# Kernel tuning notes

Measured on AMD Instinct MI355X. Metric: run time of the kernel, lower is better.

## Reference

```python
import jax, jax.numpy as jnp
import numpy as np

ASPECT_RATIOS = jnp.array([0.5, 1.0, 2.0], dtype=jnp.float32)
SCALES = jnp.array([1.0, 2.0, 4.0, 8.0, 16.0], dtype=jnp.float32)
BASE_SIZE = 16
STRIDE = 16
NEG_OVERLAP = 0.3
POS_OVERLAP = 0.7
PADDING = 0.0
RPN_BATCH = 256
RPN_FG_FRACTION = 0.5


def _mkanchors(ws, hs, x_ctr, y_ctr):
    return jnp.stack([x_ctr - 0.5 * (ws - 1), y_ctr - 0.5 * (hs - 1),
                      x_ctr + 0.5 * (ws - 1), y_ctr + 0.5 * (hs - 1)], axis=-1)


def _base_anchors():
    w = h = float(BASE_SIZE)
    x_ctr = y_ctr = 0.5 * (BASE_SIZE - 1)
    size = w * h
    size_ratios = size / ASPECT_RATIOS
    ws = jnp.round(jnp.sqrt(size_ratios))
    hs = jnp.round(ws * ASPECT_RATIOS)
    ratio_anchors = _mkanchors(ws, hs, x_ctr, y_ctr)          # (R,4)
    rw = ratio_anchors[:, 2] - ratio_anchors[:, 0] + 1
    rh = ratio_anchors[:, 3] - ratio_anchors[:, 1] + 1
    rx = ratio_anchors[:, 0] + 0.5 * (rw - 1)
    ry = ratio_anchors[:, 1] + 0.5 * (rh - 1)
    ws2 = rw[:, None] * SCALES[None, :]                        # (R,S)
    hs2 = rh[:, None] * SCALES[None, :]
    anchors = _mkanchors(ws2, hs2, rx[:, None], ry[:, None])   # (R,S,4)
    return anchors.reshape(-1, 4)                              # (A=R*S,4)


def _shifted_anchors(r, c):
    base = _base_anchors()                                     # (A,4)
    sx = jnp.arange(c, dtype=jnp.float32) * STRIDE
    sy = jnp.arange(r, dtype=jnp.float32) * STRIDE
    SX, SY = jnp.meshgrid(sx, sy)                              # (r,c)
    shifts = jnp.stack([SX.ravel(), SY.ravel(), SX.ravel(), SY.ravel()], axis=1)
    return (shifts[:, None, :] + base[None, :, :]).reshape(-1, 4)  # (K=r*c*A,4)


def _iou(a, b):
    area_a = (a[:, 2] - a[:, 0] + 1) * (a[:, 3] - a[:, 1] + 1)
    area_b = (b[:, 2] - b[:, 0] + 1) * (b[:, 3] - b[:, 1] + 1)
    iw = jnp.minimum(a[:, None, 2], b[None, :, 2]) - jnp.maximum(a[:, None, 0], b[None, :, 0]) + 1
    ih = jnp.minimum(a[:, None, 3], b[None, :, 3]) - jnp.maximum(a[:, None, 1], b[None, :, 1]) + 1
    inter = jnp.maximum(iw, 0) * jnp.maximum(ih, 0)
    return inter / (area_a[:, None] + area_b[None, :] - inter)


def _bbox_transform(ex, gt):
    ew = ex[:, 2] - ex[:, 0] + 1.0
    eh = ex[:, 3] - ex[:, 1] + 1.0
    ecx = ex[:, 0] + 0.5 * ew
    ecy = ex[:, 1] + 0.5 * eh
    gw = gt[:, 2] - gt[:, 0] + 1.0
    gh = gt[:, 3] - gt[:, 1] + 1.0
    gcx = gt[:, 0] + 0.5 * gw
    gcy = gt[:, 1] + 0.5 * gh
    return jnp.stack([(gcx - ecx) / ew, (gcy - ecy) / eh,
                      jnp.log(gw / ew), jnp.log(gh / eh)], axis=1)


def reference(target_bounding_boxes, metadata, scores):
    meta = metadata[0]
    gt = target_bounding_boxes[0]                               # (G,4)
    r, c = scores.shape[1], scores.shape[2]
    anchors = _shifted_anchors(r, c)                            # (K,4)
    K = anchors.shape[0]
    h, w = meta[0], meta[1]

    # anchors fully inside the image (padding=0); outside anchors masked
    inside = ((anchors[:, 0] >= -PADDING) & (anchors[:, 1] >= -PADDING) &
              (anchors[:, 2] < w + PADDING) & (anchors[:, 3] < h + PADDING))

    clipped = jnp.stack([jnp.clip(anchors[:, 0], 0.0, w - 1),
                         jnp.clip(anchors[:, 1], 0.0, h - 1),
                         jnp.clip(anchors[:, 2], 0.0, w - 1),
                         jnp.clip(anchors[:, 3], 0.0, h - 1)], axis=1)

    overlaps = _iou(clipped, gt)                                # (K,G)
    overlaps = jnp.where(inside[:, None], overlaps, -1.0)       # ignore outside anchors
    argmax_overlaps = jnp.argmax(overlaps, axis=1)              # best gt per anchor
    max_overlaps = jnp.max(overlaps, axis=1)
    gt_argmax = jnp.argmax(overlaps, axis=0)                    # best anchor per gt

    labels = jnp.full((K,), -1.0, dtype=jnp.float32)
    labels = jnp.where(inside & (max_overlaps < NEG_OVERLAP), 0.0, labels)
    labels = labels.at[gt_argmax].set(1.0)                      # dedup handled by .set
    labels = jnp.where(inside & (max_overlaps >= POS_OVERLAP), 1.0, labels)
    labels = jnp.where(inside, labels, -1.0)                    # unmap fill=-1

    # deterministic subsampling (original shuffles randomly): keep first-by-index
    num_fg = int(RPN_FG_FRACTION * RPN_BATCH)
    pos = labels == 1.0
    pos_rank = jnp.cumsum(pos.astype(jnp.int32))
    labels = jnp.where(pos & (pos_rank > num_fg), -1.0, labels)
    num_pos = jnp.minimum(pos.sum(), num_fg)
    num_bg = RPN_BATCH - num_pos
    neg = labels == 0.0
    neg_rank = jnp.cumsum(neg.astype(jnp.int32))
    labels = jnp.where(neg & (neg_rank > num_bg), -1.0, labels)

    matched_gt = gt[argmax_overlaps]                            # (K,4) gather
    bbox_targets = _bbox_transform(clipped, matched_gt)
    bbox_targets = jnp.where(inside[:, None], bbox_targets, 0.0)  # unmap fill=0

    return anchors[None], bbox_targets[None], labels[None]


def setup_inputs() -> dict:
    key = jax.random.key(0)
    k1, k2 = jax.random.split(key)
    H = W = 1600
    G = 100
    r = c = H // STRIDE                                          # 100
    A = 15                                                       # 3 ratios * 5 scales
    xy = jax.random.uniform(k1, (G, 2), minval=0.0, maxval=1400.0)
    wh = jax.random.uniform(k2, (G, 2), minval=16.0, maxval=200.0)
    gt = jnp.concatenate([xy, xy + wh], axis=1)[None]            # (1,G,4)
    metadata = jnp.array([[float(H), float(W), 1.0]], dtype=jnp.float32)
    scores = jnp.zeros((1, r, c, A), dtype=jnp.float32)          # only shape is used
    return {"target_bounding_boxes": gt, "metadata": metadata, "scores": scores}
```

## Files before the change

kernel.cpp:

```cpp
#include <hip/hip_runtime.h>
#include <math.h>


#define NUM_A 15
#define NUM_FG 128
#define RPN_BATCH 256
#define BLOCK 256
#define MAXG 256
#define SCAN_T 1024

__device__ __forceinline__ void base_anchor(int a, float& bx1, float& by1,
                                            float& bx2, float& by2) {
    const float RW[3] = {23.f, 16.f, 11.f};
    const float RH[3] = {12.f, 16.f, 22.f};
    int i = a / 5;
    int j = a - i * 5;
    float sc = (float)(1 << j);
    float w = RW[i] * sc;
    float h = RH[i] * sc;
    bx1 = 7.5f - 0.5f * (w - 1.f);
    by1 = 7.5f - 0.5f * (h - 1.f);
    bx2 = 7.5f + 0.5f * (w - 1.f);
    by2 = 7.5f + 0.5f * (h - 1.f);
}

__device__ __forceinline__ void anchor_coords(int k, int c, float& x1, float& y1,
                                              float& x2, float& y2) {
    int a = k % NUM_A;
    int p = k / NUM_A;
    int xi = p % c;
    int yi = p / c;
    float bx1, by1, bx2, by2;
    base_anchor(a, bx1, by1, bx2, by2);
    float sx = (float)xi * 16.f;
    float sy = (float)yi * 16.f;
    x1 = sx + bx1;  y1 = sy + by1;
    x2 = sx + bx2;  y2 = sy + by2;
}

__device__ __forceinline__ unsigned long long packvk(float v, int k) {
    unsigned u = __float_as_uint(v);
    u = (u & 0x80000000u) ? ~u : (u | 0x80000000u);
    return ((unsigned long long)u << 32) | (unsigned)(~k);
}

__global__ void __launch_bounds__(BLOCK) k_main(
        const float* __restrict__ gt, const float* __restrict__ meta,
        float* __restrict__ out_anch, float* __restrict__ out_bb,
        float* __restrict__ out_lab, int* __restrict__ posc, int* __restrict__ negc,
        unsigned long long* __restrict__ bestg, int K, int c, int G) {
    __shared__ float4 s_gt[MAXG];
    __shared__ unsigned long long s_best[MAXG];
    __shared__ int swp[4], swn[4];
    int tid = threadIdx.x;
    const float4* gtv = (const float4*)gt;
    for (int g = tid; g < G; g += BLOCK) {
        s_gt[g] = gtv[g];
        s_best[g] = 0ULL;
    }
    __syncthreads();

    int k = blockIdx.x * BLOCK + tid;
    bool valid = (k < K);
    float h = meta[0], w = meta[1];
    float wm1 = __fsub_rn(w, 1.f), hm1 = __fsub_rn(h, 1.f);

    float x1, y1, x2, y2;
    anchor_coords(k, c, x1, y1, x2, y2);
    if (valid) ((float4*)out_anch)[k] = make_float4(x1, y1, x2, y2);
    bool inside = (x1 >= 0.f) && (y1 >= 0.f) && (x2 < w) && (y2 < h);

    float cx1 = fminf(fmaxf(x1, 0.f), wm1);
    float cy1 = fminf(fmaxf(y1, 0.f), hm1);
    float cx2 = fminf(fmaxf(x2, 0.f), wm1);
    float cy2 = fminf(fmaxf(y2, 0.f), hm1);
    float area_a = __fmul_rn(__fadd_rn(__fsub_rn(cx2, cx1), 1.f),
                             __fadd_rn(__fsub_rn(cy2, cy1), 1.f));

    float maxv = -2.f;
    int arg = 0;
    if (valid && inside) {
        for (int g = 0; g < G; ++g) {
            float4 gb = gtv[g];
            float gw = __fadd_rn(__fsub_rn(gb.z, gb.x), 1.f);
            float gh = __fadd_rn(__fsub_rn(gb.w, gb.y), 1.f);
            float areab = __fmul_rn(gw, gh);
            float iw = __fadd_rn(__fsub_rn(fminf(cx2, gb.z), fmaxf(cx1, gb.x)), 1.f);
            float ih = __fadd_rn(__fsub_rn(fminf(cy2, gb.w), fmaxf(cy1, gb.y)), 1.f);
            float inter = __fmul_rn(fmaxf(iw, 0.f), fmaxf(ih, 0.f));
            float v = 0.f;
            if (inter > 0.f) {
                float denom = __fsub_rn(__fadd_rn(area_a, areab), inter);
                v = __fdiv_rn(inter, denom);
                atomicMax(&s_best[g], packvk(v, k));
            }
            if (v > maxv) { maxv = v; arg = g; }
        }
    }
    __syncthreads();
    for (int g = tid; g < G; g += BLOCK)
        if (s_best[g] != 0ULL) atomicMax(&bestg[g], s_best[g]);

    float labf = -1.f;
    if (valid) {
        float t0 = 0.f, t1 = 0.f, t2 = 0.f, t3 = 0.f;
        if (inside) {
            labf = (maxv >= 0.7f) ? 1.f : (maxv < 0.3f ? 0.f : -1.f);
            float4 gb = s_gt[arg];
            float ew  = __fadd_rn(__fsub_rn(cx2, cx1), 1.f);
            float eh  = __fadd_rn(__fsub_rn(cy2, cy1), 1.f);
            float ecx = __fadd_rn(cx1, __fmul_rn(0.5f, ew));
            float ecy = __fadd_rn(cy1, __fmul_rn(0.5f, eh));
            float gw  = __fadd_rn(__fsub_rn(gb.z, gb.x), 1.f);
            float gh  = __fadd_rn(__fsub_rn(gb.w, gb.y), 1.f);
            float gcx = __fadd_rn(gb.x, __fmul_rn(0.5f, gw));
            float gcy = __fadd_rn(gb.y, __fmul_rn(0.5f, gh));
            t0 = __fdiv_rn(__fsub_rn(gcx, ecx), ew);
            t1 = __fdiv_rn(__fsub_rn(gcy, ecy), eh);
            t2 = logf(__fdiv_rn(gw, ew));
            t3 = logf(__fdiv_rn(gh, eh));
        }
        ((float4*)out_bb)[k] = make_float4(t0, t1, t2, t3);
        out_lab[k] = labf;
    }

    bool pos = valid && (labf == 1.f);
    bool neg = valid && (labf == 0.f);
    unsigned long long bp = __ballot(pos ? 1 : 0);
    unsigned long long bn = __ballot(neg ? 1 : 0);
    int lane = tid & 63, wid = tid >> 6;
    if (lane == 0) { swp[wid] = __popcll(bp); swn[wid] = __popcll(bn); }
    __syncthreads();
    if (tid == 0) {
        posc[blockIdx.x] = swp[0] + swp[1] + swp[2] + swp[3];
        negc[blockIdx.x] = swn[0] + swn[1] + swn[2] + swn[3];
    }
}

__global__ void __launch_bounds__(SCAN_T) k_scan1(
        const unsigned long long* __restrict__ bestg, float* __restrict__ lab,
        int* __restrict__ posc, int* __restrict__ negc, int* __restrict__ numbg,
        int NB, int G) {
    __shared__ int sp[SCAN_T], sn[SCAN_T];
    __shared__ int s_k[MAXG];
    int tid = threadIdx.x;
    sp[tid] = (tid < NB) ? posc[tid] : 0;
    sn[tid] = (tid < NB) ? negc[tid] : 0;

    int kstar = -1;
    if (tid < G) {
        unsigned long long u = bestg[tid];
        if (u != 0ULL)
            kstar = (int)(~(unsigned)(u & 0xffffffffu));
    }
    if (tid < MAXG) s_k[tid] = kstar;
    __syncthreads();
    bool mine = (kstar >= 0);
    if (mine) {
        for (int j = 0; j < tid; ++j)
            if (s_k[j] == kstar) { mine = false; break; }
    }
    if (mine) {
        float oldl = lab[kstar];
        if (oldl != 1.f) {
            lab[kstar] = 1.f;
            int b = kstar / BLOCK;
            atomicAdd(&sp[b], 1);
            if (oldl == 0.f) atomicAdd(&sn[b], -1);
        }
    }
    __syncthreads();
    int op = sp[tid], on = sn[tid];
    int vp = op, vn = on;
    for (int off = 1; off < SCAN_T; off <<= 1) {
        int ap = 0, an = 0;
        if (tid >= off) { ap = sp[tid - off]; an = sn[tid - off]; }
        __syncthreads();
        vp += ap; vn += an;
        sp[tid] = vp; sn[tid] = vn;
        __syncthreads();
    }
    if (tid < NB) { posc[tid] = vp - op; negc[tid] = vn - on; }
    if (tid == 0) {
        int total_pos = sp[SCAN_T - 1];
        int np = total_pos < NUM_FG ? total_pos : NUM_FG;
        numbg[0] = RPN_BATCH - np;
    }
}

__global__ void __launch_bounds__(BLOCK) k_apply(
        float* __restrict__ lab, const int* __restrict__ posoff,
        const int* __restrict__ negoff, const int* __restrict__ numbg, int K) {
    __shared__ int swp[4], swn[4];
    int tid = threadIdx.x;
    int lane = tid & 63, wid = tid >> 6;
    unsigned long long lm = (1ULL << lane) - 1ULL;
    int k = blockIdx.x * BLOCK + tid;
    float lv = (k < K) ? lab[k] : -1.f;
    bool pos = (k < K) && (lv == 1.f);
    bool neg = (k < K) && (lv == 0.f);
    unsigned long long bp = __ballot(pos ? 1 : 0);
    unsigned long long bn = __ballot(neg ? 1 : 0);
    if (lane == 0) { swp[wid] = __popcll(bp); swn[wid] = __popcll(bn); }
    __syncthreads();
    int poff = 0, noff = 0;
    for (int wv = 0; wv < 4; ++wv)
        if (wv < wid) { poff += swp[wv]; noff += swn[wv]; }
    int prank = posoff[blockIdx.x] + poff + __popcll(bp & lm) + 1;
    int nrank = negoff[blockIdx.x] + noff + __popcll(bn & lm) + 1;
    int nb = numbg[0];
    if (pos && prank > NUM_FG) lab[k] = -1.f;
    if (neg && nrank > nb)     lab[k] = -1.f;
}

extern "C" void kernel_launch(void* const* d_in, const int* in_sizes, int n_in,
                              void* d_out, int out_size, void* d_ws, size_t ws_size,
                              hipStream_t stream) {
    const float* gt   = (const float*)d_in[0];
    const float* meta = (const float*)d_in[1];
    int G  = in_sizes[0] / 4;
    int rc = in_sizes[2] / NUM_A;
    int c = 1;
    while ((long long)(c + 1) * (c + 1) <= (long long)rc) ++c;
    int K  = rc * NUM_A;
    int NB = (K + BLOCK - 1) / BLOCK;

    float* out      = (float*)d_out;
    float* out_anch = out;
    float* out_bb   = out + (size_t)4 * K;
    float* out_lab  = out + (size_t)8 * K;

    unsigned long long* bestg = (unsigned long long*)d_ws;
    int* posc  = (int*)(bestg + MAXG);
    int* negc  = posc + SCAN_T;
    int* numbg = negc + SCAN_T;

    hipMemsetAsync(bestg, 0, MAXG * sizeof(unsigned long long), stream);
    hipLaunchKernelGGL(k_main, dim3(NB), dim3(BLOCK), 0, stream,
                       gt, meta, out_anch, out_bb, out_lab, posc, negc, bestg, K, c, G);
    hipLaunchKernelGGL(k_scan1, dim3(1), dim3(SCAN_T), 0, stream,
                       bestg, out_lab, posc, negc, numbg, NB, G);
    hipLaunchKernelGGL(k_apply, dim3(NB), dim3(BLOCK), 0, stream,
                       out_lab, posc, negc, numbg, K);
}
```

Measured before the change: 111.2 us.

## Fuse three kernels into one cooperative kernel with grid syncs and wave-reduced atomics

Merges the IoU/label kernel, the single-block scan and the apply kernel into one cooperative launch that separates phases with grid-wide syncs. This removes two kernel launches and their inter-kernel gaps. It also reduces the per-GT best-anchor atomics with a wavefront shuffle max before one shared atomic per wave, and the scan now runs with 256 threads over 4 elements each. The trade-off is cooperative-launch overhead, a grid-wide barrier cost, and the requirement that all ~586 blocks be co-resident.

```diff
diff --git a/kernel.cpp b/kernel.cpp
--- a/kernel.cpp
+++ b/kernel.cpp
@@ -1,5 +1,8 @@
 #include <hip/hip_runtime.h>
+#include <hip/hip_cooperative_groups.h>
 #include <math.h>
+
+namespace cg = cooperative_groups;
 
 
 #define NUM_A 15
@@ -7,7 +10,7 @@
 #define RPN_BATCH 256
 #define BLOCK 256
 #define MAXG 256
-#define SCAN_T 1024
+#define MAXNB 1024
 
 __device__ __forceinline__ void base_anchor(int a, float& bx1, float& by1,
                                             float& bx2, float& by2) {
@@ -44,20 +47,26 @@
     return ((unsigned long long)u << 32) | (unsigned)(~k);
 }
 
-__global__ void __launch_bounds__(BLOCK) k_main(
+__global__ void __launch_bounds__(BLOCK) k_fused(
         const float* __restrict__ gt, const float* __restrict__ meta,
         float* __restrict__ out_anch, float* __restrict__ out_bb,
-        float* __restrict__ out_lab, int* __restrict__ posc, int* __restrict__ negc,
-        unsigned long long* __restrict__ bestg, int K, int c, int G) {
+        float* __restrict__ out_lab,
+        int* __restrict__ posc, int* __restrict__ negc,
+        unsigned long long* __restrict__ bestg, int* __restrict__ numbg,
+        int K, int c, int G, int NB) {
     __shared__ float4 s_gt[MAXG];
     __shared__ unsigned long long s_best[MAXG];
     __shared__ int swp[4], swn[4];
+    __shared__ int s_p[MAXNB], s_n[MAXNB];
+    __shared__ int s_cp[BLOCK], s_cn[BLOCK];
+    __shared__ int s_k[MAXG];
+
+    cg::grid_group gg = cg::this_grid();
     int tid = threadIdx.x;
+    int lane = tid & 63, wid = tid >> 6;
     const float4* gtv = (const float4*)gt;
-    for (int g = tid; g < G; g += BLOCK) {
-        s_gt[g] = gtv[g];
-        s_best[g] = 0ULL;
-    }
+    for (int g = tid; g < G; g += BLOCK) s_gt[g] = gtv[g];
+    for (int g = tid; g < MAXG; g += BLOCK) s_best[g] = 0ULL;
     __syncthreads();
 
     int k = blockIdx.x * BLOCK + tid;
@@ -69,6 +78,7 @@
     anchor_coords(k, c, x1, y1, x2, y2);
     if (valid) ((float4*)out_anch)[k] = make_float4(x1, y1, x2, y2);
     bool inside = (x1 >= 0.f) && (y1 >= 0.f) && (x2 < w) && (y2 < h);
+    bool act_anchor = valid && inside;
 
     float cx1 = fminf(fmaxf(x1, 0.f), wm1);
     float cy1 = fminf(fmaxf(y1, 0.f), hm1);
@@ -79,7 +89,7 @@
 
     float maxv = -2.f;
     int arg = 0;
-    if (valid && inside) {
+    if (__any(act_anchor ? 1 : 0)) {
         for (int g = 0; g < G; ++g) {
             float4 gb = gtv[g];
             float gw = __fadd_rn(__fsub_rn(gb.z, gb.x), 1.f);
@@ -88,13 +98,23 @@
             float iw = __fadd_rn(__fsub_rn(fminf(cx2, gb.z), fmaxf(cx1, gb.x)), 1.f);
             float ih = __fadd_rn(__fsub_rn(fminf(cy2, gb.w), fmaxf(cy1, gb.y)), 1.f);
             float inter = __fmul_rn(fmaxf(iw, 0.f), fmaxf(ih, 0.f));
+            bool act = act_anchor && (inter > 0.f);
             float v = 0.f;
-            if (inter > 0.f) {
+            unsigned long long pk = 0ULL;
+            if (act) {
                 float denom = __fsub_rn(__fadd_rn(area_a, areab), inter);
                 v = __fdiv_rn(inter, denom);
-                atomicMax(&s_best[g], packvk(v, k));
+                pk = packvk(v, k);
             }
-            if (v > maxv) { maxv = v; arg = g; }
+            if (__any(act ? 1 : 0)) {
+                #pragma unroll
+                for (int off = 1; off < 64; off <<= 1) {
+                    unsigned long long o = __shfl_xor(pk, off, 64);
+                    if (o > pk) pk = o;
+                }
+                if (lane == 0 && pk != 0ULL) atomicMax(&s_best[g], pk);
+            }
+            if (act_anchor && v > maxv) { maxv = v; arg = g; }
         }
     }
     __syncthreads();
@@ -128,89 +148,90 @@
     bool neg = valid && (labf == 0.f);
     unsigned long long bp = __ballot(pos ? 1 : 0);
     unsigned long long bn = __ballot(neg ? 1 : 0);
-    int lane = tid & 63, wid = tid >> 6;
     if (lane == 0) { swp[wid] = __popcll(bp); swn[wid] = __popcll(bn); }
     __syncthreads();
     if (tid == 0) {
         posc[blockIdx.x] = swp[0] + swp[1] + swp[2] + swp[3];
         negc[blockIdx.x] = swn[0] + swn[1] + swn[2] + swn[3];
     }
-}
-
-__global__ void __launch_bounds__(SCAN_T) k_scan1(
-        const unsigned long long* __restrict__ bestg, float* __restrict__ lab,
-        int* __restrict__ posc, int* __restrict__ negc, int* __restrict__ numbg,
-        int NB, int G) {
-    __shared__ int sp[SCAN_T], sn[SCAN_T];
-    __shared__ int s_k[MAXG];
-    int tid = threadIdx.x;
-    sp[tid] = (tid < NB) ? posc[tid] : 0;
-    sn[tid] = (tid < NB) ? negc[tid] : 0;
-
-    int kstar = -1;
-    if (tid < G) {
-        unsigned long long u = bestg[tid];
-        if (u != 0ULL)
-            kstar = (int)(~(unsigned)(u & 0xffffffffu));
-    }
-    if (tid < MAXG) s_k[tid] = kstar;
-    __syncthreads();
-    bool mine = (kstar >= 0);
-    if (mine) {
-        for (int j = 0; j < tid; ++j)
-            if (s_k[j] == kstar) { mine = false; break; }
-    }
-    if (mine) {
-        float oldl = lab[kstar];
-        if (oldl != 1.f) {
-            lab[kstar] = 1.f;
-            int b = kstar / BLOCK;
-            atomicAdd(&sp[b], 1);
-            if (oldl == 0.f) atomicAdd(&sn[b], -1);
-        }
-    }
-    __syncthreads();
-    int op = sp[tid], on = sn[tid];
-    int vp = op, vn = on;
-    for (int off = 1; off < SCAN_T; off <<= 1) {
-        int ap = 0, an = 0;
-        if (tid >= off) { ap = sp[tid - off]; an = sn[tid - off]; }
-        __syncthreads();
-        vp += ap; vn += an;
-        sp[tid] = vp; sn[tid] = vn;
-        __syncthreads();
-    }
-    if (tid < NB) { posc[tid] = vp - op; negc[tid] = vn - on; }
-    if (tid == 0) {
-        int total_pos = sp[SCAN_T - 1];
-        int np = total_pos < NUM_FG ? total_pos : NUM_FG;
-        numbg[0] = RPN_BATCH - np;
-    }
-}
-
-__global__ void __launch_bounds__(BLOCK) k_apply(
-        float* __restrict__ lab, const int* __restrict__ posoff,
-        const int* __restrict__ negoff, const int* __restrict__ numbg, int K) {
-    __shared__ int swp[4], swn[4];
-    int tid = threadIdx.x;
-    int lane = tid & 63, wid = tid >> 6;
-    unsigned long long lm = (1ULL << lane) - 1ULL;
-    int k = blockIdx.x * BLOCK + tid;
-    float lv = (k < K) ? lab[k] : -1.f;
-    bool pos = (k < K) && (lv == 1.f);
-    bool neg = (k < K) && (lv == 0.f);
-    unsigned long long bp = __ballot(pos ? 1 : 0);
-    unsigned long long bn = __ballot(neg ? 1 : 0);
-    if (lane == 0) { swp[wid] = __popcll(bp); swn[wid] = __popcll(bn); }
-    __syncthreads();
-    int poff = 0, noff = 0;
-    for (int wv = 0; wv < 4; ++wv)
-        if (wv < wid) { poff += swp[wv]; noff += swn[wv]; }
-    int prank = posoff[blockIdx.x] + poff + __popcll(bp & lm) + 1;
-    int nrank = negoff[blockIdx.x] + noff + __popcll(bn & lm) + 1;
-    int nb = numbg[0];
-    if (pos && prank > NUM_FG) lab[k] = -1.f;
-    if (neg && nrank > nb)     lab[k] = -1.f;
+
+    __threadfence();
+    gg.sync();
+
+    if (blockIdx.x == 0) {
+        for (int i = tid; i < MAXNB; i += BLOCK) {
+            s_p[i] = (i < NB) ? posc[i] : 0;
+            s_n[i] = (i < NB) ? negc[i] : 0;
+        }
+        int kstar = -1;
+        if (tid < G) {
+            unsigned long long u = bestg[tid];
+            if (u != 0ULL)
+                kstar = (int)(~(unsigned)(u & 0xffffffffu));
+        }
+        if (tid < MAXG) s_k[tid] = kstar;
+        __syncthreads();
+        bool mine = (kstar >= 0);
+        if (mine) {
+            for (int j = 0; j < tid; ++j)
+                if (s_k[j] == kstar) { mine = false; break; }
+        }
+        if (mine) {
+            float oldl = out_lab[kstar];
+            if (oldl != 1.f) {
+                out_lab[kstar] = 1.f;
+                atomicAdd(&s_p[kstar / BLOCK], 1);
+                if (oldl == 0.f) atomicAdd(&s_n[kstar / BLOCK], -1);
+            }
+        }
+        __syncthreads();
+        int base = tid * 4;
+        int p0 = s_p[base], p1 = s_p[base + 1], p2 = s_p[base + 2], p3 = s_p[base + 3];
+        int n0 = s_n[base], n1 = s_n[base + 1], n2 = s_n[base + 2], n3 = s_n[base + 3];
+        int sump = p0 + p1 + p2 + p3, sumn = n0 + n1 + n2 + n3;
+        s_cp[tid] = sump; s_cn[tid] = sumn;
+        __syncthreads();
+        int vp = sump, vn = sumn;
+        for (int off = 1; off < BLOCK; off <<= 1) {
+            int ap = 0, an = 0;
+            if (tid >= off) { ap = s_cp[tid - off]; an = s_cn[tid - off]; }
+            __syncthreads();
+            vp += ap; vn += an;
+            s_cp[tid] = vp; s_cn[tid] = vn;
+            __syncthreads();
+        }
+        int ep = vp - sump, en = vn - sumn;
+        posc[base] = ep; ep += p0; posc[base + 1] = ep; ep += p1;
+        posc[base + 2] = ep; ep += p2; posc[base + 3] = ep;
+        negc[base] = en; en += n0; negc[base + 1] = en; en += n1;
+        negc[base + 2] = en; en += n2; negc[base + 3] = en;
+        if (tid == BLOCK - 1) {
+            int np = vp < NUM_FG ? vp : NUM_FG;
+            numbg[0] = RPN_BATCH - np;
+        }
+    }
+
+    __threadfence();
+    gg.sync();
+    __syncthreads();
+
+    {
+        unsigned long long lm = (1ULL << lane) - 1ULL;
+        float lv = valid ? out_lab[k] : -1.f;
+        bool posf = valid && (lv == 1.f);
+        bool negf = valid && (lv == 0.f);
+        unsigned long long bp2 = __ballot(posf ? 1 : 0);
+        unsigned long long bn2 = __ballot(negf ? 1 : 0);
+        if (lane == 0) { swp[wid] = __popcll(bp2); swn[wid] = __popcll(bn2); }
+        __syncthreads();
+        int poff = 0, noff = 0;
+        for (int wv = 0; wv < wid; ++wv) { poff += swp[wv]; noff += swn[wv]; }
+        int prank = posc[blockIdx.x] + poff + __popcll(bp2 & lm) + 1;
+        int nrank = negc[blockIdx.x] + noff + __popcll(bn2 & lm) + 1;
+        int nb = numbg[0];
+        if (posf && prank > NUM_FG) out_lab[k] = -1.f;
+        if (negf && nrank > nb)     out_lab[k] = -1.f;
+    }
 }
 
 extern "C" void kernel_launch(void* const* d_in, const int* in_sizes, int n_in,
@@ -232,14 +253,13 @@
 
     unsigned long long* bestg = (unsigned long long*)d_ws;
     int* posc  = (int*)(bestg + MAXG);
-    int* negc  = posc + SCAN_T;
-    int* numbg = negc + SCAN_T;
+    int* negc  = posc + MAXNB;
+    int* numbg = negc + MAXNB;
 
     hipMemsetAsync(bestg, 0, MAXG * sizeof(unsigned long long), stream);
-    hipLaunchKernelGGL(k_main, dim3(NB), dim3(BLOCK), 0, stream,
-                       gt, meta, out_anch, out_bb, out_lab, posc, negc, bestg, K, c, G);
-    hipLaunchKernelGGL(k_scan1, dim3(1), dim3(SCAN_T), 0, stream,
-                       bestg, out_lab, posc, negc, numbg, NB, G);
-    hipLaunchKernelGGL(k_apply, dim3(NB), dim3(BLOCK), 0, stream,
-                       out_lab, posc, negc, numbg, K);
-}
+    void* args[] = { (void*)&gt, (void*)&meta, (void*)&out_anch, (void*)&out_bb,
+                     (void*)&out_lab, (void*)&posc, (void*)&negc, (void*)&bestg,
+                     (void*)&numbg, (void*)&K, (void*)&c, (void*)&G, (void*)&NB };
+    hipLaunchCooperativeKernel((const void*)k_fused, dim3(NB), dim3(BLOCK),
+                               args, 0, stream);
+}
```

New measurement: 289.1 us. 2.6x slower.
